# Kernel optimization log

Hardware: AMD Instinct MI355X
Metric: run time of the kernel (lower is better)

The kernel has to match this reference:

```python
import jax, jax.numpy as jnp
import numpy as np

P_MIN = 0.8        # minimum cumulative probability mass kept per row
THRESHOLD = 1e-10  # drop matches with probability below this
EPS = 1e-6         # distance clamp (matches dist.clamp(min=1e-6) in backward)

B, N, M, D = 4, 4096, 4096, 3


def setup_inputs() -> dict:
    key = jax.random.key(0)
    kx, ky = jax.random.split(key)
    x = jax.random.normal(kx, (B, N, D), dtype=jnp.float32)
    y = jax.random.normal(ky, (B, M, D), dtype=jnp.float32)
    return {"x": x, "y": y}


def _pairwise_dist(x, y):
    # ||x_i - y_j|| via Gram trick; avoids materializing [B,N,M,D] diff tensor.
    sq = (
        jnp.sum(x * x, axis=-1)[:, :, None]
        + jnp.sum(y * y, axis=-1)[:, None, :]
        - 2.0 * jnp.einsum("bnd,bmd->bnm", x, y)
    )
    return jnp.sqrt(jnp.maximum(sq, EPS * EPS))  # [B, N, M]


def _sparse_match_weights(d):
    # Row-wise soft matching probabilities over targets j.
    p = jax.nn.softmax(-d, axis=-1)  # [B, N, M]
    # Keep the most-probable entries per row until cumulative mass reaches P_MIN
    # (the dense, jit-friendly equivalent of the COO compaction in the kernel).
    order = jnp.argsort(-p, axis=-1)
    p_sorted = jnp.take_along_axis(p, order, axis=-1)
    csum = jnp.cumsum(p_sorted, axis=-1)
    keep_sorted = (csum - p_sorted) < P_MIN  # include entry that crosses P_MIN
    inv = jnp.argsort(order, axis=-1)
    keep = jnp.take_along_axis(keep_sorted, inv, axis=-1)
    return jnp.where(keep & (p > THRESHOLD), p, 0.0)  # sparse COO values, dense layout


def reference(x, y):
    d = _pairwise_dist(x, y)                     # [B, N, M]
    w = jax.lax.stop_gradient(_sparse_match_weights(d))  # weights are constants in bwd
    loss = jnp.sum(w * d)                        # scalar matching loss
    return loss
```

## Files before the change

kernel.cpp:

```cpp
#include <hip/hip_runtime.h>


#define MCOLS 4096
#define KPT   64
#define WPB   4
#define P_MIN 0.8f

template <int CTRL, int RM, int BM, bool BC>
__device__ __forceinline__ float dpp_mov0(float x) {
    return __int_as_float(__builtin_amdgcn_update_dpp(
        0, __float_as_int(x), CTRL, RM, BM, BC));
}
__device__ __forceinline__ float dppSum(float v) {
    v += dpp_mov0<0x111, 0xF, 0xF, true >(v);
    v += dpp_mov0<0x112, 0xF, 0xF, true >(v);
    v += dpp_mov0<0x114, 0xF, 0xF, true >(v);
    v += dpp_mov0<0x118, 0xF, 0xF, true >(v);
    v += dpp_mov0<0x142, 0xA, 0xF, false>(v);
    v += dpp_mov0<0x143, 0xC, 0xF, false>(v);
    return __int_as_float(__builtin_amdgcn_readlane(__float_as_int(v), 63));
}
__device__ __forceinline__ float dppMax(float v) {
    v = fmaxf(v, dpp_mov0<0x111, 0xF, 0xF, true >(v));
    v = fmaxf(v, dpp_mov0<0x112, 0xF, 0xF, true >(v));
    v = fmaxf(v, dpp_mov0<0x114, 0xF, 0xF, true >(v));
    v = fmaxf(v, dpp_mov0<0x118, 0xF, 0xF, true >(v));
    v = fmaxf(v, dpp_mov0<0x142, 0xA, 0xF, false>(v));
    v = fmaxf(v, dpp_mov0<0x143, 0xC, 0xF, false>(v));
    return __int_as_float(__builtin_amdgcn_readlane(__float_as_int(v), 63));
}

__global__ __launch_bounds__(WPB * 64) void apml_row_wave(
        const float* __restrict__ x, const float* __restrict__ y,
        float* __restrict__ out) {
    __shared__ __align__(16) float scomp[WPB * 256];
    __shared__ float wacc[WPB];

    const int tid  = threadIdx.x;
    const int wid  = tid >> 6;
    const int lane = tid & 63;
    const int row  = blockIdx.x * WPB + wid;
    const int b    = row >> 12;

    const float x0 = x[row * 3 + 0];
    const float x1 = x[row * 3 + 1];
    const float x2 = x[row * 3 + 2];
    const float* yb = y + (size_t)b * MCOLS * 3;

    float p[KPT];
    float zl = 0.0f, pml = 0.0f;
    #pragma unroll
    for (int k = 0; k < KPT; ++k) {
        const int j = k * 64 + lane;
        const float y0 = yb[j * 3 + 0];
        const float y1 = yb[j * 3 + 1];
        const float y2 = yb[j * 3 + 2];
        const float dx = x0 - y0, dy = x1 - y1, dz = x2 - y2;
        const float sq = fmaxf(dx * dx + dy * dy + dz * dz, 1e-12f);
        const float pk = __expf(-sqrtf(sq));
        p[k] = pk;
        zl  += pk;
        pml  = fmaxf(pml, pk);
    }
    const float Z    = dppSum(zl);
    const float pmax = dppMax(pml);
    const float target = P_MIN * Z;
    const float pTop = __uint_as_float(__float_as_uint(pmax) + 1u);

    float ssl = 0.0f, ssh = pTop;
    {
        float eGl = 16.0f * dppSum(p[0] + p[1] + p[2] + p[3]);
        float eGh = 0.0f;
        for (int it = 0; it < 5; ++it) {
            float s;
            if (it & 1) {
                s = 0.5f * (ssl + ssh);
            } else {
                const float den = fmaxf(eGl - eGh, 1e-30f);
                s = ssl + (ssh - ssl) * ((eGl - target) / den);
            }
            if (!(s > ssl && s < ssh)) s = 0.5f * (ssl + ssh);
            if (!(s > ssl && s < ssh)) break;
            float m = 0.0f;
            #pragma unroll
            for (int q = 0; q < 4; ++q) m += (p[q] >= s) ? p[q] : 0.0f;
            m = 16.0f * dppSum(m);
            if (m >= target) { ssl = s; eGl = m; }
            else             { ssh = s; eGh = m; }
        }
    }

    float sl = 0.0f, sh = pTop;
    float Gl = Z,    Gh = 0.0f;
    int   Cl = MCOLS, Ch = 0;

    for (int it = 0; it < 12 && (Cl - Ch) > 256; ++it) {
        float s;
        if      (it == 0) s = ssl;
        else if (it == 1) s = ssh;
        else if (it & 1)  s = 0.5f * (sl + sh);
        else {
            const float den = fmaxf(Gl - Gh, 1e-30f);
            s = sl + (sh - sl) * ((Gl - target) / den);
        }
        if (!(s > sl && s < sh)) s = 0.5f * (sl + sh);
        if (!(s > sl && s < sh)) break;

        float m = 0.0f;
        int   c = 0;
        #pragma unroll
        for (int k = 0; k < KPT; ++k) {
            const bool ge = (p[k] >= s);
            m += ge ? p[k] : 0.0f;
            c += (int)__popcll(__ballot(ge));
        }
        m = dppSum(m);
        if (m >= target) { sl = s; Gl = m; Cl = c; }
        else             { sh = s; Gh = m; Ch = c; }
    }

    int C = 0;
    #pragma unroll
    for (int k = 0; k < KPT; ++k) {
        const bool band = (p[k] >= sl) && (p[k] < sh);
        const unsigned long long mk = __ballot(band);
        if (band) {
            const unsigned mlo = (unsigned)mk, mhi = (unsigned)(mk >> 32);
            const int within = __builtin_amdgcn_mbcnt_hi(
                                   mhi, __builtin_amdgcn_mbcnt_lo(mlo, 0));
            const int pos = C + within;
            if (pos < 256) scomp[wid * 256 + pos] = p[k];
        }
        C += (int)__popcll(mk);
    }
    __builtin_amdgcn_s_waitcnt(0);
    float cp[4];
    bool  cv[4];
    #pragma unroll
    for (int q = 0; q < 4; ++q) {
        const int idx = q * 64 + lane;
        cv[q] = (idx < C) && (idx < 256);
        cp[q] = cv[q] ? scomp[wid * 256 + idx] : 0.0f;
    }

    float pstar, mb = 0.0f;
    int   cnt = 1;
    bool  haveTie;

    if (C > 256) {
        pstar = (sl > 0.0f) ? __uint_as_float(__float_as_uint(sl) - 1u) : 0.0f;
        haveTie = false;
    } else {
        float lo_s = sl, hi_s = sh, lo_G = Gl, hi_G = Gh;
        int   lo_C = Cl, hi_C = Ch;
        for (int it = 0; it < 10 && (lo_C - hi_C) > 2; ++it) {
            float s;
            if (it & 1) {
                s = 0.5f * (lo_s + hi_s);
            } else {
                const float den = fmaxf(lo_G - hi_G, 1e-30f);
                s = lo_s + (hi_s - lo_s) * ((lo_G - target) / den);
            }
            if (!(s > lo_s && s < hi_s)) s = 0.5f * (lo_s + hi_s);
            if (!(s > lo_s && s < hi_s)) break;

            float m = 0.0f;
            int   c = Ch;
            #pragma unroll
            for (int q = 0; q < 4; ++q) {
                const bool ge = cv[q] && (cp[q] >= s);
                m += ge ? cp[q] : 0.0f;
                c += (int)__popcll(__ballot(ge));
            }
            m = Gh + dppSum(m);
            if (m >= target) { lo_s = s; lo_G = m; lo_C = c; }
            else             { hi_s = s; hi_G = m; hi_C = c; }
        }

        float scur = hi_s, M = hi_G;
        bool ok = false;
        pstar = lo_s;
        for (int e = 0; e < 16; ++e) {
            float vl = 0.0f;
            #pragma unroll
            for (int q = 0; q < 4; ++q)
                vl = fmaxf(vl, (cv[q] && cp[q] < scur) ? cp[q] : 0.0f);
            const float v = dppMax(vl);
            if (!(v > 0.0f)) break;
            int cvn = 0;
            #pragma unroll
            for (int q = 0; q < 4; ++q)
                cvn += (int)__popcll(__ballot(cv[q] && (cp[q] == v)));
            const float Mn = M + v * (float)cvn;
            if (Mn >= target) { pstar = v; mb = M; cnt = cvn; ok = true; break; }
            M = Mn; scur = v;
        }
        haveTie = ok;
        if (!ok) {
            pstar = (lo_s > 0.0f) ? __uint_as_float(__float_as_uint(lo_s) - 1u)
                                  : 0.0f;
        }
    }

    float spd = 0.0f;
    #pragma unroll
    for (int k = 0; k < KPT; ++k) {
        const float t = (p[k] > pstar) ? p[k] : 1.0f;
        spd += t * (-__logf(t));
    }
    spd = dppSum(spd);

    if (lane == 0) {
        float tie = 0.0f;
        if (haveTie) {
            const float R = (target - mb) / pstar;
            int q = (int)ceilf(R);
            if (q < 1) q = 1;
            if (q > cnt) q = cnt;
            tie = (float)q * pstar * (-__logf(pstar));
        }
        wacc[wid] = (spd + tie) / Z;
    }
    __syncthreads();
    if (tid == 0) {
        atomicAdd(out, wacc[0] + wacc[1] + wacc[2] + wacc[3]);
    }
}

extern "C" void kernel_launch(void* const* d_in, const int* in_sizes, int n_in,
                              void* d_out, int out_size, void* d_ws, size_t ws_size,
                              hipStream_t stream) {
    const float* x = (const float*)d_in[0];
    const float* y = (const float*)d_in[1];
    float* out = (float*)d_out;

    const int nrows = in_sizes[0] / 3;
    const int nblocks = nrows / WPB;

    hipMemsetAsync(out, 0, sizeof(float), stream);
    apml_row_wave<<<nblocks, WPB * 64, 0, stream>>>(x, y, out);
}
```

Before: 167.9 us.

## Compute kept-entropy sum by complement and widen compaction buffer to 512

The kernel now accumulates sum(p*d) over the whole row while computing distances. The kept-mass term is then obtained by subtracting two pieces: the below-band entropy, folded into the compaction pass, and a small sum over the compacted band. This removes the separate final 64-element log pass. The compaction capacity grows from 256 to 512 entries per wave, and the bisection is seeded with a widened bracket after one fewer pre-estimate iteration, to reduce full-row search passes. The trade-off is more registers for the 8-slot band arrays and more shared memory, plus a small float cancellation error from the subtraction.

```diff
diff --git a/kernel.cpp b/kernel.cpp
--- a/kernel.cpp
+++ b/kernel.cpp
@@ -5,6 +5,7 @@
 #define KPT   64
 #define WPB   4
 #define P_MIN 0.8f
+#define CAP   512
 
 template <int CTRL, int RM, int BM, bool BC>
 __device__ __forceinline__ float dpp_mov0(float x) {
@@ -33,7 +34,7 @@
 __global__ __launch_bounds__(WPB * 64) void apml_row_wave(
         const float* __restrict__ x, const float* __restrict__ y,
         float* __restrict__ out) {
-    __shared__ __align__(16) float scomp[WPB * 256];
+    __shared__ __align__(16) float scomp[WPB * CAP];
     __shared__ float wacc[WPB];
 
     const int tid  = threadIdx.x;
@@ -48,7 +49,7 @@
     const float* yb = y + (size_t)b * MCOLS * 3;
 
     float p[KPT];
-    float zl = 0.0f, pml = 0.0f;
+    float zl = 0.0f, pml = 0.0f, sal = 0.0f;
     #pragma unroll
     for (int k = 0; k < KPT; ++k) {
         const int j = k * 64 + lane;
@@ -57,21 +58,24 @@
         const float y2 = yb[j * 3 + 2];
         const float dx = x0 - y0, dy = x1 - y1, dz = x2 - y2;
         const float sq = fmaxf(dx * dx + dy * dy + dz * dz, 1e-12f);
-        const float pk = __expf(-sqrtf(sq));
+        const float dd = sqrtf(sq);
+        const float pk = __expf(-dd);
         p[k] = pk;
         zl  += pk;
         pml  = fmaxf(pml, pk);
-    }
-    const float Z    = dppSum(zl);
-    const float pmax = dppMax(pml);
-    const float target = P_MIN * Z;
+        sal  = fmaf(pk, dd, sal);
+    }
+    const float Z       = dppSum(zl);
+    const float pmax    = dppMax(pml);
+    const float spd_all = dppSum(sal);
+    const float target  = P_MIN * Z;
     const float pTop = __uint_as_float(__float_as_uint(pmax) + 1u);
 
     float ssl = 0.0f, ssh = pTop;
     {
         float eGl = 16.0f * dppSum(p[0] + p[1] + p[2] + p[3]);
         float eGh = 0.0f;
-        for (int it = 0; it < 5; ++it) {
+        for (int it = 0; it < 4; ++it) {
             float s;
             if (it & 1) {
                 s = 0.5f * (ssl + ssh);
@@ -89,15 +93,18 @@
             else             { ssh = s; eGh = m; }
         }
     }
+    const float wbw = ssh - ssl;
+    const float seed_lo = fmaxf(ssl - wbw, 0.0f);
+    const float seed_hi = fminf(ssh + wbw, pTop);
 
     float sl = 0.0f, sh = pTop;
     float Gl = Z,    Gh = 0.0f;
     int   Cl = MCOLS, Ch = 0;
 
-    for (int it = 0; it < 12 && (Cl - Ch) > 256; ++it) {
+    for (int it = 0; it < 12 && (Cl - Ch) > CAP; ++it) {
         float s;
-        if      (it == 0) s = ssl;
-        else if (it == 1) s = ssh;
+        if      (it == 0) s = seed_lo;
+        else if (it == 1) s = seed_hi;
         else if (it & 1)  s = 0.5f * (sl + sh);
         else {
             const float den = fmaxf(Gl - Gh, 1e-30f);
@@ -120,34 +127,40 @@
     }
 
     int C = 0;
+    float slo = 0.0f;
     #pragma unroll
     for (int k = 0; k < KPT; ++k) {
-        const bool band = (p[k] >= sl) && (p[k] < sh);
+        const float pv = p[k];
+        const bool below = (pv < sl);
+        const float t = below ? pv : 1.0f;
+        slo -= t * __logf(t);
+        const bool band = !below && (pv < sh);
         const unsigned long long mk = __ballot(band);
         if (band) {
             const unsigned mlo = (unsigned)mk, mhi = (unsigned)(mk >> 32);
             const int within = __builtin_amdgcn_mbcnt_hi(
                                    mhi, __builtin_amdgcn_mbcnt_lo(mlo, 0));
             const int pos = C + within;
-            if (pos < 256) scomp[wid * 256 + pos] = p[k];
+            if (pos < CAP) scomp[wid * CAP + pos] = pv;
         }
         C += (int)__popcll(mk);
     }
+    const float S_lo = dppSum(slo);
     __builtin_amdgcn_s_waitcnt(0);
-    float cp[4];
-    bool  cv[4];
-    #pragma unroll
-    for (int q = 0; q < 4; ++q) {
+    float cp[8];
+    bool  cv[8];
+    #pragma unroll
+    for (int q = 0; q < 8; ++q) {
         const int idx = q * 64 + lane;
-        cv[q] = (idx < C) && (idx < 256);
-        cp[q] = cv[q] ? scomp[wid * 256 + idx] : 0.0f;
+        cv[q] = (idx < C) && (idx < CAP);
+        cp[q] = cv[q] ? scomp[wid * CAP + idx] : 0.0f;
     }
 
     float pstar, mb = 0.0f;
     int   cnt = 1;
     bool  haveTie;
 
-    if (C > 256) {
+    if (C > CAP) {
         pstar = (sl > 0.0f) ? __uint_as_float(__float_as_uint(sl) - 1u) : 0.0f;
         haveTie = false;
     } else {
@@ -167,7 +180,7 @@
             float m = 0.0f;
             int   c = Ch;
             #pragma unroll
-            for (int q = 0; q < 4; ++q) {
+            for (int q = 0; q < 8; ++q) {
                 const bool ge = cv[q] && (cp[q] >= s);
                 m += ge ? cp[q] : 0.0f;
                 c += (int)__popcll(__ballot(ge));
@@ -183,13 +196,13 @@
         for (int e = 0; e < 16; ++e) {
             float vl = 0.0f;
             #pragma unroll
-            for (int q = 0; q < 4; ++q)
+            for (int q = 0; q < 8; ++q)
                 vl = fmaxf(vl, (cv[q] && cp[q] < scur) ? cp[q] : 0.0f);
             const float v = dppMax(vl);
             if (!(v > 0.0f)) break;
             int cvn = 0;
             #pragma unroll
-            for (int q = 0; q < 4; ++q)
+            for (int q = 0; q < 8; ++q)
                 cvn += (int)__popcll(__ballot(cv[q] && (cp[q] == v)));
             const float Mn = M + v * (float)cvn;
             if (Mn >= target) { pstar = v; mb = M; cnt = cvn; ok = true; break; }
@@ -202,13 +215,15 @@
         }
     }
 
-    float spd = 0.0f;
-    #pragma unroll
-    for (int k = 0; k < KPT; ++k) {
-        const float t = (p[k] > pstar) ? p[k] : 1.0f;
-        spd += t * (-__logf(t));
-    }
-    spd = dppSum(spd);
+    float sble = 0.0f;
+    #pragma unroll
+    for (int q = 0; q < 8; ++q) {
+        const float t = (cv[q] && (cp[q] <= pstar)) ? cp[q] : 1.0f;
+        sble -= t * __logf(t);
+    }
+    const float S_band_le = dppSum(sble);
+
+    const float spd = spd_all - S_lo - S_band_le;
 
     if (lane == 0) {
         float tie = 0.0f;
```

New measurement: 188.3 us. 1.12x slower.
